# Kernel tuning notes

Hardware: AMD Instinct MI355X
Metric: run time of the kernel (lower is better)

Reference implementation:

```python
import jax, jax.numpy as jnp
import numpy as np

DIM = 1024
HEADS = 16
HEAD_DIM = DIM // HEADS
B, S, L0, L1 = 2, 2048, 2048, 2048


def setup_inputs() -> dict:
    key = jax.random.key(0)
    ks = jax.random.split(key, 10)
    sc = DIM ** -0.5
    return {
        "query": jax.random.normal(ks[0], (B, S, DIM), jnp.float32),
        "l0_keys": jax.random.normal(ks[1], (B, L0, DIM), jnp.float32),
        "l0_values": jax.random.normal(ks[2], (B, L0, DIM), jnp.float32),
        "l1_keys": jax.random.normal(ks[3], (B, L1, DIM), jnp.float32),
        "l1_values": jax.random.normal(ks[4], (B, L1, DIM), jnp.float32),
        "l0_mask": jax.random.randint(ks[5], (S, L0), 0, 2, jnp.int32),
        "Wq": jax.random.normal(ks[6], (DIM, DIM), jnp.float32) * sc,
        "bq": jnp.zeros((DIM,), jnp.float32),
        "Wo": jax.random.normal(ks[7], (DIM, DIM), jnp.float32) * sc,
        "bo": jnp.zeros((DIM,), jnp.float32),
        "gate": jnp.asarray(0.0, jnp.float32),
    }


def reference(query, l0_keys, l0_values, l1_keys, l1_values, l0_mask, Wq, bq, Wo, bo, gate):
    b, s, d = query.shape
    h, hd = HEADS, HEAD_DIM
    scale = hd ** -0.5
    # q: [B,H,S,hd]
    q = (query @ Wq.T + bq).reshape(b, s, h, hd).transpose(0, 2, 1, 3)

    def attend(keys, values, mask):
        L = keys.shape[1]
        k = keys.reshape(b, L, h, hd)
        v = values.reshape(b, L, h, hd)
        scores = jnp.einsum("bhsd,blhd->bhsl", q, k) * scale
        if mask is not None:
            scores = jnp.where(mask[None, None] == 0, -jnp.inf, scores)
        w = jax.nn.softmax(scores, axis=-1)  # [B,H,S,L]
        out = jnp.einsum("bhsl,blhd->bshd", w, v)  # [B,S,H,hd]
        return out, w.mean(axis=1)

    out0, a0 = attend(l0_keys, l0_values, l0_mask)
    out1, a1 = attend(l1_keys, l1_values, None)
    g = jax.nn.sigmoid(gate)
    out = (g * out0 + (1.0 - g) * out1).reshape(b, s, d)
    out = out @ Wo.T + bo
    return out, a0, a1
```

## Files before the change

kernel.cpp:

```cpp
#include <hip/hip_runtime.h>

#define DIM   1024
#define HEADS 16
#define HD    64
#define BB    2
#define SS    2048
#define LLL   2048
#define LOG2E 1.4426950408889634f

typedef __bf16 bf16x8 __attribute__((ext_vector_type(8)));
typedef __bf16 bf16x4v __attribute__((ext_vector_type(4)));
typedef float  f32x4  __attribute__((ext_vector_type(4)));
typedef short  s16x4  __attribute__((ext_vector_type(4)));
typedef unsigned short u16;

static __device__ __forceinline__ u16 f2b(float x) {
  unsigned u = __float_as_uint(x);
  u += 0x7fffu + ((u >> 16) & 1u);
  return (u16)(u >> 16);
}
static __device__ __forceinline__ float b2f(u16 u) {
  return __uint_as_float(((unsigned)u) << 16);
}
static __device__ __forceinline__ f32x4 mfma32(bf16x8 a, bf16x8 b, f32x4 c) {
  return __builtin_amdgcn_mfma_f32_16x16x32_bf16(a, b, c, 0, 0, 0);
}

static __device__ __forceinline__ void gload_lds16(const void* g, void* lds_uniform_base) {
#if __has_builtin(__builtin_amdgcn_global_load_lds)
  __builtin_amdgcn_global_load_lds(
      (const __attribute__((address_space(1))) unsigned int*)g,
      (__attribute__((address_space(3))) unsigned int*)lds_uniform_base, 16, 0, 0);
#else
  const int l = threadIdx.x & 63;
  ((uint4*)lds_uniform_base)[l] = ((const uint4*)g)[0];
#endif
}

__global__ void prep(const float* __restrict__ a, const float* __restrict__ b,
                     const float* __restrict__ c, u16* __restrict__ da,
                     u16* __restrict__ db_, u16* __restrict__ dc,
                     const int* __restrict__ mask, unsigned* __restrict__ mbits,
                     int na4, int nb4, int ncvt) {
  int i = blockIdx.x * blockDim.x + threadIdx.x;
  if (i < ncvt) {
    const float* s; u16* d; int j = i;
    if (j < na4) { s = a; d = da; }
    else if ((j -= na4) < nb4) { s = b; d = db_; }
    else { j -= nb4; s = c; d = dc; }
    float4 f = ((const float4*)s)[j];
    ushort4 o;
    o.x = f2b(f.x); o.y = f2b(f.y); o.z = f2b(f.z); o.w = f2b(f.w);
    ((ushort4*)d)[j] = o;
  } else {
    int j = i - ncvt;
    const int* src = mask + (size_t)j * 32;
    unsigned bm = 0;
#pragma unroll
    for (int jj = 0; jj < 8; ++jj) {
      int4 m = ((const int4*)src)[jj];
      bm |= (m.x != 0 ? 1u : 0u) << (jj * 4 + 0);
      bm |= (m.y != 0 ? 1u : 0u) << (jj * 4 + 1);
      bm |= (m.z != 0 ? 1u : 0u) << (jj * 4 + 2);
      bm |= (m.w != 0 ? 1u : 0u) << (jj * 4 + 3);
    }
    mbits[j] = bm;
  }
}

__global__ __launch_bounds__(256) void pack_k(const float* __restrict__ k0,
                                              const float* __restrict__ k1,
                                              u16* __restrict__ Kfrag) {
  const float SCK = 0.125f * LOG2E;
  const int w = threadIdx.x >> 6, l = threadIdx.x & 63, g = l >> 4, li = l & 15;
  const int lt = blockIdx.x * 4 + w, h = blockIdx.y, z = blockIdx.z;
  const int lay = z >> 1, b = z & 1;
  const float* src = (lay ? k1 : k0) + (size_t)b * LLL * DIM;
  u16* dst = Kfrag + ((((size_t)z * HEADS + h) * 32 + lt) * 8) * 512;
#pragma unroll
  for (int c = 0; c < 8; ++c) {
    int mt = c >> 1, kk = c & 1;
    const float* p = &src[(size_t)(lt * 64 + mt * 16 + li) * DIM + h * 64 + kk * 32 + g * 8];
    float4 f0 = *(const float4*)p;
    float4 f1 = *(const float4*)(p + 4);
    u16 u[8] = {f2b(f0.x * SCK), f2b(f0.y * SCK), f2b(f0.z * SCK), f2b(f0.w * SCK),
                f2b(f1.x * SCK), f2b(f1.y * SCK), f2b(f1.z * SCK), f2b(f1.w * SCK)};
    *(uint4*)&dst[c * 512 + l * 8] = *(uint4*)u;
  }
}

__global__ __launch_bounds__(256) void pack_v(const float* __restrict__ v0,
                                              const float* __restrict__ v1,
                                              u16* __restrict__ Vfrag) {
  __shared__ u16 T[64][72];
  const int lt = blockIdx.x, h = blockIdx.y, z = blockIdx.z;
  const int lay = z >> 1, b = z & 1;
  const float* v = (lay ? v1 : v0) + (size_t)b * LLL * DIM;
  const int t = threadIdx.x;
  {
    int r = t >> 2, c16 = (t & 3) * 16;
    const float* src = &v[(size_t)(lt * 64 + r) * DIM + h * 64 + c16];
#pragma unroll
    for (int i = 0; i < 4; ++i) {
      float4 f = *(const float4*)&src[i * 4];
      T[r][c16 + i * 4 + 0] = f2b(f.x);
      T[r][c16 + i * 4 + 1] = f2b(f.y);
      T[r][c16 + i * 4 + 2] = f2b(f.z);
      T[r][c16 + i * 4 + 3] = f2b(f.w);
    }
  }
  __syncthreads();
  u16* dst = Vfrag + ((((size_t)z * HEADS + h) * 32 + lt) * 8) * 512;
  {
    int lane = t & 63, g = lane >> 4, li = lane & 15;
#pragma unroll
    for (int cc = 0; cc < 2; ++cc) {
      int c = (t >> 6) + cc * 4;
      int pair = c >> 2, dt = c & 3;
      u16 u[8];
#pragma unroll
      for (int j = 0; j < 4; ++j) u[j]     = T[pair * 32 + 4 * g + j][dt * 16 + li];
#pragma unroll
      for (int j = 0; j < 4; ++j) u[4 + j] = T[pair * 32 + 16 + 4 * g + j][dt * 16 + li];
      *(uint4*)&dst[c * 512 + lane * 8] = *(uint4*)u;
    }
  }
}

template<int MODE>
__global__ __launch_bounds__(256) void gemm_nt(const u16* __restrict__ A,
                                               const u16* __restrict__ Bt,
                                               const float* __restrict__ bias,
                                               void* __restrict__ Cv,
                                               int M, int N, int K) {
  __shared__ u16 As[2][128][64];
  __shared__ u16 Bs[2][64][64];
  const int t = threadIdx.x;
  const int w = t >> 6, l = t & 63, g = l >> 4, li = l & 15;
  const int m0 = blockIdx.y * 128, n0 = blockIdx.x * 64;
  const int slotL = w * 64 + l;
  const int rA = slotL >> 3, cA = ((slotL & 7) * 8) ^ ((rA & 7) * 8);

  auto stageAB = [&](int buf, int kt) {
#pragma unroll
    for (int s = 0; s < 4; ++s) {
      int r = rA + s * 32;
      gload_lds16(&A[(size_t)(m0 + r) * K + kt + cA], &As[buf][0][0] + (s * 256 + w * 64) * 8);
    }
#pragma unroll
    for (int s = 0; s < 2; ++s) {
      int r = rA + s * 32;
      gload_lds16(&Bt[(size_t)(n0 + r) * K + kt + cA], &Bs[buf][0][0] + (s * 256 + w * 64) * 8);
    }
  };

  f32x4 acc[2][4] = {};
  stageAB(0, 0);
  __syncthreads();
  int cur = 0;
  for (int kt = 0; kt < K; kt += 64) {
    if (kt + 64 < K) stageAB(cur ^ 1, kt + 64);
#pragma unroll
    for (int kk = 0; kk < 2; ++kk) {
      bf16x8 a[2], bfr[4];
#pragma unroll
      for (int mi = 0; mi < 2; ++mi) {
        int ra = w * 32 + mi * 16 + li;
        a[mi] = *(const bf16x8*)&As[cur][ra][(kk * 32 + g * 8) ^ ((ra & 7) << 3)];
      }
#pragma unroll
      for (int ni = 0; ni < 4; ++ni) {
        int rb = ni * 16 + li;
        bfr[ni] = *(const bf16x8*)&Bs[cur][rb][(kk * 32 + g * 8) ^ ((rb & 7) << 3)];
      }
#pragma unroll
      for (int mi = 0; mi < 2; ++mi)
#pragma unroll
        for (int ni = 0; ni < 4; ++ni)
          acc[mi][ni] = mfma32(a[mi], bfr[ni], acc[mi][ni]);
    }
    __syncthreads();
    cur ^= 1;
  }
#pragma unroll
  for (int mi = 0; mi < 2; ++mi)
#pragma unroll
    for (int ni = 0; ni < 4; ++ni)
#pragma unroll
      for (int v = 0; v < 4; ++v) {
        int rr = m0 + w * 32 + mi * 16 + g * 4 + v;
        int cc = n0 + ni * 16 + li;
        float val = acc[mi][ni][v] + bias[cc];
        if (MODE == 1) {
          ((float*)Cv)[(size_t)rr * N + cc] = val;
        } else {
          int b = rr >> 11, q = rr & 2047;
          int qt = q >> 5, n = (q >> 4) & 1, liq = q & 15;
          int h = (cc >> 6) & 15, kk2 = (cc >> 5) & 1, gp = (cc >> 3) & 3, j = cc & 7;
          size_t base = ((((size_t)b * HEADS + h) * 64 + qt) * 4 + n * 2 + kk2) * 512;
          ((u16*)Cv)[base + (size_t)(gp * 16 + liq) * 8 + j] = f2b(val);
        }
      }
}

template<int MASKED>
static __device__ __forceinline__ void attn_pv_body(int z, int h, int qt, int w, int l,
                                                    const u16* __restrict__ Qfrag,
                                                    const u16* __restrict__ Kfrag,
                                                    const u16* __restrict__ Vfrag,
                                                    const unsigned* __restrict__ mbits,
                                                    u16* __restrict__ out01,
                                                    float* __restrict__ db,
                                                    u16* __restrict__ KV) {
  const int g = l >> 4, li = l & 15;
  const int b = z & 1;
  const u16* kfh = Kfrag + (size_t)(z * HEADS + h) * (32 * 8 * 512);
  const u16* vfh = Vfrag + (size_t)(z * HEADS + h) * (32 * 8 * 512);
  const u16* qfh = Qfrag + (((size_t)(b * HEADS + h) * 64 + qt) * 4) * 512;

  bf16x8 qf[2][2];
#pragma unroll
  for (int n = 0; n < 2; ++n)
#pragma unroll
    for (int kk = 0; kk < 2; ++kk)
      qf[n][kk] = *(const bf16x8*)&qfh[(n * 2 + kk) * 512 + l * 8];

  const unsigned* mrow0 = MASKED ? mbits + (size_t)(qt * 32 + li) * (LLL / 32) : nullptr;
  const unsigned* mrow1 = MASKED ? mrow0 + 16 * (LLL / 32) : nullptr;
  const int shb = 4 * g;
  bf16x8 ones8;
#pragma unroll
  for (int j = 0; j < 8; ++j) ones8[j] = __builtin_bit_cast(__bf16, (u16)0x3F80);

  auto stage = [&](int buf, int lt) {
    const u16* kfl = kfh + (size_t)lt * 4096;
    const u16* vfl = vfh + (size_t)lt * 4096;
#pragma unroll
    for (int i2 = 0; i2 < 2; ++i2) {
      int f = w * 2 + i2;
      const u16* gsrc = (f < 8 ? kfl + f * 512 : vfl + (f - 8) * 512) + l * 8;
      gload_lds16(gsrc, (char*)KV + buf * 16384 + f * 1024);
    }
  };

  f32x4 dacc[2] = {};
  f32x4 oacc[4][2] = {};

  stage(0, 0);
  __syncthreads();
  int cur = 0;
  for (int lt = 0; lt < 32; ++lt) {
    if (lt + 1 < 32) stage(cur ^ 1, lt + 1);
    unsigned mw[2][2];
    if (MASKED) {
      mw[0][0] = mrow0[lt * 2]; mw[0][1] = mrow0[lt * 2 + 1];
      mw[1][0] = mrow1[lt * 2]; mw[1][1] = mrow1[lt * 2 + 1];
    }
    const u16* Ks = KV + cur * 8192;
    const u16* Vs = Ks + 4096;

    auto qk = [&](f32x4 (&s)[2], int mt) {
      bf16x8 k0 = *(const bf16x8*)&Ks[(mt * 2 + 0) * 512 + l * 8];
      bf16x8 k1 = *(const bf16x8*)&Ks[(mt * 2 + 1) * 512 + l * 8];
      f32x4 zz = {};
      __builtin_amdgcn_s_setprio(1);
      s[0] = mfma32(k0, qf[0][0], zz);
      s[0] = mfma32(k1, qf[0][1], s[0]);
      s[1] = mfma32(k0, qf[1][0], zz);
      s[1] = mfma32(k1, qf[1][1], s[1]);
      __builtin_amdgcn_s_setprio(0);
    };
    auto sm = [&](f32x4 (&s)[2], int mt, s16x4 (&wpk)[2]) {
#pragma unroll
      for (int n = 0; n < 2; ++n) {
        unsigned mm = MASKED ? (mw[n][mt >> 1] >> ((mt & 1) * 16 + shb)) : 0u;
        f32x4 ev;
#pragma unroll
        for (int v = 0; v < 4; ++v) {
          float e = __builtin_amdgcn_exp2f(s[n][v]);
          if (MASKED) {
            int spread = ((int)(mm << (31 - v))) >> 31;
            e = __uint_as_float(__float_as_uint(e) & (unsigned)spread);
          }
          ev[v] = e;
        }
        bf16x4v wb = __builtin_convertvector(ev, bf16x4v);
        wpk[n] = __builtin_bit_cast(s16x4, wb);
      }
    };
    auto pv_pair = [&](s16x4 (&w0)[2], s16x4 (&w1)[2], int pair) {
      bf16x8 w8[2];
#pragma unroll
      for (int n = 0; n < 2; ++n) {
        bf16x4v a0 = __builtin_bit_cast(bf16x4v, w0[n]);
        bf16x4v a1 = __builtin_bit_cast(bf16x4v, w1[n]);
        w8[n] = __builtin_shufflevector(a0, a1, 0, 1, 2, 3, 4, 5, 6, 7);
      }
      __builtin_amdgcn_s_setprio(1);
      dacc[0] = mfma32(ones8, w8[0], dacc[0]);
      dacc[1] = mfma32(ones8, w8[1], dacc[1]);
#pragma unroll
      for (int dt = 0; dt < 4; ++dt) {
        bf16x8 vf = *(const bf16x8*)&Vs[(pair * 4 + dt) * 512 + l * 8];
#pragma unroll
        for (int n = 0; n < 2; ++n)
          oacc[dt][n] = mfma32(vf, w8[n], oacc[dt][n]);
      }
      __builtin_amdgcn_s_setprio(0);
    };

    f32x4 sA[2], sB[2];
    s16x4 wA[2], wB[2];
    qk(sA, 0); qk(sB, 1);
    sm(sA, 0, wA);
    qk(sA, 2);
    sm(sB, 1, wB);
    pv_pair(wA, wB, 0);
    qk(sB, 3);
    sm(sA, 2, wA);
    sm(sB, 3, wB);
    pv_pair(wA, wB, 1);
    __syncthreads();
    cur ^= 1;
  }
  float dinv[2];
  dinv[0] = 1.0f / dacc[0][0];
  dinv[1] = 1.0f / dacc[1][0];
  if (l < 16) {
    db[(size_t)(z * HEADS + h) * SS + qt * 32 + li]      = -__log2f(dacc[0][0]);
    db[(size_t)(z * HEADS + h) * SS + qt * 32 + 16 + li] = -__log2f(dacc[1][0]);
  }
  u16* ob = out01 + (size_t)z * SS * DIM;
#pragma unroll
  for (int dt = 0; dt < 4; ++dt)
#pragma unroll
    for (int n = 0; n < 2; ++n) {
      f32x4 o = oacc[dt][n] * dinv[n];
      ushort4 us;
      us.x = f2b(o[0]); us.y = f2b(o[1]); us.z = f2b(o[2]); us.w = f2b(o[3]);
      *(ushort4*)&ob[((size_t)(qt * 32 + n * 16 + li)) * DIM + h * HD + dt * 16 + 4 * g] = us;
    }
}

__global__ __launch_bounds__(512, 4) void attn_pv(const u16* __restrict__ Qfrag,
                                                  const u16* __restrict__ Kfrag,
                                                  const u16* __restrict__ Vfrag,
                                                  const unsigned* __restrict__ mbits,
                                                  u16* __restrict__ out01,
                                                  float* __restrict__ db) {
  __shared__ u16 KV[2][8192];
  const int flat = blockIdx.x;
  const int xcd = flat & 7, i = flat >> 3;
  const int k = i >> 3, qg = i & 7;
  const int zh = xcd + 8 * k;
  const int z = zh >> 4, h = zh & 15;
  const int w = threadIdx.x >> 6, l = threadIdx.x & 63;
  const int qt = qg * 8 + w;
  if (z < 2) attn_pv_body<1>(z, h, qt, w, l, Qfrag, Kfrag, Vfrag, mbits, out01, db, &KV[0][0]);
  else       attn_pv_body<0>(z, h, qt, w, l, Qfrag, Kfrag, Vfrag, mbits, out01, db, &KV[0][0]);
}

template<int MASKED>
static __device__ __forceinline__ void amean_body(int z, int qt, int lt, int w, int l,
                                                  const u16* __restrict__ Qfrag,
                                                  const u16* __restrict__ Kfrag,
                                                  const unsigned* __restrict__ mbits,
                                                  const float* __restrict__ db,
                                                  float* __restrict__ aout,
                                                  u16* __restrict__ KS) {
  const int g = l >> 4, li = l & 15;
  const int b = z & 1;

  unsigned mw[2][2];
  if (MASKED) {
    const unsigned* m0 = mbits + (size_t)(qt * 32 + li) * (LLL / 32) + lt * 2;
    const unsigned* m1 = m0 + 16 * (LLL / 32);
    mw[0][0] = m0[0]; mw[0][1] = m0[1];
    mw[1][0] = m1[0]; mw[1][1] = m1[1];
  }
  const u16* qf_base = Qfrag + (((size_t)(b * HEADS) * 64 + qt) * 4) * 512 + l * 8;
  const float* dbb = db + (size_t)(z * HEADS) * SS + qt * 32 + li;

  auto stageK = [&](int buf, int h) {
    const u16* kfh = Kfrag + ((((size_t)(z * HEADS + h)) * 32 + lt) * 8) * 512;
    gload_lds16(kfh + w * 512 + l * 8, (char*)KS + buf * 8192 + w * 1024);
  };

  f32x4 asum[4][2] = {};
  stageK(0, 0);
  __syncthreads();
#pragma unroll 2
  for (int h = 0; h < HEADS; ++h) {
    if (h + 1 < HEADS) stageK((h + 1) & 1, h + 1);
    float l2[2];
    l2[0] = dbb[(size_t)h * SS];
    l2[1] = dbb[(size_t)h * SS + 16];
    bf16x8 qf[2][2];
#pragma unroll
    for (int n = 0; n < 2; ++n)
#pragma unroll
      for (int kk = 0; kk < 2; ++kk)
        qf[n][kk] = *(const bf16x8*)&qf_base[(size_t)h * (64 * 4 * 512) + (n * 2 + kk) * 512];
    const u16* Ks = KS + (h & 1) * 4096;
#pragma unroll
    for (int mt = 0; mt < 4; ++mt) {
      bf16x8 k0 = *(const bf16x8*)&Ks[(mt * 2 + 0) * 512 + l * 8];
      bf16x8 k1 = *(const bf16x8*)&Ks[(mt * 2 + 1) * 512 + l * 8];
#pragma unroll
      for (int n = 0; n < 2; ++n) {
        f32x4 s;
        __builtin_amdgcn_s_setprio(1);
        f32x4 zz = {};
        s = mfma32(k0, qf[n][0], zz);
        s = mfma32(k1, qf[n][1], s);
        __builtin_amdgcn_s_setprio(0);
        unsigned mm = MASKED ? (mw[n][mt >> 1] >> ((mt & 1) * 16 + 4 * g)) : 0u;
#pragma unroll
        for (int v = 0; v < 4; ++v) {
          float e = __builtin_amdgcn_exp2f(s[v] + l2[n]);
          if (MASKED) {
            int spread = ((int)(mm << (31 - v))) >> 31;
            e = __uint_as_float(__float_as_uint(e) & (unsigned)spread);
          }
          asum[mt][n][v] += e;
        }
      }
    }
    __syncthreads();
  }
  float* ab = aout + (size_t)z * SS * LLL;
#pragma unroll
  for (int mt = 0; mt < 4; ++mt)
#pragma unroll
    for (int n = 0; n < 2; ++n) {
      f32x4 o = asum[mt][n] * 0.0625f;
      f32x4* dst = (f32x4*)&ab[(size_t)(qt * 32 + n * 16 + li) * LLL + lt * 64 + mt * 16 + 4 * g];
      __builtin_nontemporal_store(o, dst);
    }
}

__global__ __launch_bounds__(512, 4) void amean(const u16* __restrict__ Qfrag,
                                                const u16* __restrict__ Kfrag,
                                                const unsigned* __restrict__ mbits,
                                                const float* __restrict__ db,
                                                float* __restrict__ aout) {
  __shared__ u16 KS[2][4096];
  const int flat = blockIdx.x;
  const int xcd = flat & 7, i = flat >> 3;
  const int k = i >> 3, qg = i & 7;
  const int zlt = xcd + 8 * k;
  const int z = zlt >> 5, lt = zlt & 31;
  const int w = threadIdx.x >> 6, l = threadIdx.x & 63;
  const int qt = qg * 8 + w;
  if (z < 2) amean_body<1>(z, qt, lt, w, l, Qfrag, Kfrag, mbits, db, aout, &KS[0][0]);
  else       amean_body<0>(z, qt, lt, w, l, Qfrag, Kfrag, mbits, db, aout, &KS[0][0]);
}

__global__ void merge_kernel(const u16* __restrict__ o01,
                             const float* __restrict__ gate,
                             u16* __restrict__ merged) {
  int i = blockIdx.x * blockDim.x + threadIdx.x;
  float gv = gate[0];
  float g = 1.0f / (1.0f + __builtin_amdgcn_exp2f(-gv * LOG2E));
  const size_t n = (size_t)BB * SS * DIM;
  ushort4 a = ((const ushort4*)o01)[i];
  ushort4 c = ((const ushort4*)(o01 + n))[i];
  ushort4 o;
  o.x = f2b(g * b2f(a.x) + (1.f - g) * b2f(c.x));
  o.y = f2b(g * b2f(a.y) + (1.f - g) * b2f(c.y));
  o.z = f2b(g * b2f(a.z) + (1.f - g) * b2f(c.z));
  o.w = f2b(g * b2f(a.w) + (1.f - g) * b2f(c.w));
  ((ushort4*)merged)[i] = o;
}

extern "C" void kernel_launch(void* const* d_in, const int* in_sizes, int n_in,
                              void* d_out, int out_size, void* d_ws, size_t ws_size,
                              hipStream_t stream) {
  const float* query = (const float*)d_in[0];
  const float* k0f   = (const float*)d_in[1];
  const float* v0f   = (const float*)d_in[2];
  const float* k1f   = (const float*)d_in[3];
  const float* v1f   = (const float*)d_in[4];
  const int*   mask  = (const int*)d_in[5];
  const float* Wqf   = (const float*)d_in[6];
  const float* bq    = (const float*)d_in[7];
  const float* Wof   = (const float*)d_in[8];
  const float* bo    = (const float*)d_in[9];
  const float* gate  = (const float*)d_in[10];
  float* out = (float*)d_out;

  const size_t nQ = (size_t)BB * SS * DIM;
  const size_t nW = (size_t)DIM * DIM;

  char* ws = (char*)d_ws;
  size_t off = 0;
  auto alloc = [&](size_t bytes) -> char* {
    char* p = ws + off;
    off += (bytes + 255) & ~(size_t)255;
    return p;
  };
  u16*      queryb  = (u16*)alloc(nQ * 2);
  u16*      wqb     = (u16*)alloc(nW * 2);
  u16*      wob     = (u16*)alloc(nW * 2);
  u16*      Qfrag   = (u16*)alloc(nQ * 2);
  u16*      Kfrag   = (u16*)alloc((size_t)2 * nQ * 2);
  u16*      Vfrag   = (u16*)alloc((size_t)2 * nQ * 2);
  unsigned* mbits   = (unsigned*)alloc((size_t)SS * (LLL / 32) * 4);
  float*    db      = (float*)alloc((size_t)4 * HEADS * SS * 4);
  u16*      out01   = (u16*)alloc((size_t)2 * nQ * 2);
  u16*      mergedb = queryb;

  {
    int na4 = (int)(nQ / 4), nb4 = (int)(nW / 4);
    int ncvt = na4 + 2 * nb4;
    int nmask = SS * (LLL / 32);
    prep<<<dim3((ncvt + nmask) / 256), dim3(256), 0, stream>>>(
        query, Wqf, Wof, queryb, wqb, wob, mask, mbits, na4, nb4, ncvt);
  }

  pack_k<<<dim3(LLL / 64 / 4, HEADS, 4), dim3(256), 0, stream>>>(k0f, k1f, Kfrag);
  pack_v<<<dim3(LLL / 64, HEADS, 4), dim3(256), 0, stream>>>(v0f, v1f, Vfrag);

  gemm_nt<2><<<dim3(DIM / 64, (BB * SS) / 128), dim3(256), 0, stream>>>(
      queryb, wqb, bq, (void*)Qfrag, BB * SS, DIM, DIM);

  attn_pv<<<dim3(512), dim3(512), 0, stream>>>(Qfrag, Kfrag, Vfrag, mbits, out01, db);

  amean<<<dim3(1024), dim3(512), 0, stream>>>(Qfrag, Kfrag, mbits, db, out + nQ);

  merge_kernel<<<dim3((int)(nQ / 4 / 256)), dim3(256), 0, stream>>>(out01, gate, mergedb);

  gemm_nt<1><<<dim3(DIM / 64, (BB * SS) / 128), dim3(256), 0, stream>>>(
      mergedb, wob, bo, (void*)out, BB * SS, DIM, DIM);
}
```

Before: 213.1 us.

## Simplify amean softmax: store reciprocal denom, mask once at store, smaller blocks

The attention kernel now stores the reciprocal of the softmax denominator instead of a negative log2, so amean computes exp2(s)*dinv with an FMA instead of adding a bias inside the exp. Because the mask is the same for every head, it is applied once to the final mean at store time rather than per head inside the loop. The mask-word registers and setprio calls are dropped. amean also moves to 256-thread blocks with twice as many blocks, each wave staging two K fragments, to change occupancy and scheduling.

```diff
diff --git a/kernel.cpp b/kernel.cpp
--- a/kernel.cpp
+++ b/kernel.cpp
@@ -327,8 +327,8 @@
   dinv[0] = 1.0f / dacc[0][0];
   dinv[1] = 1.0f / dacc[1][0];
   if (l < 16) {
-    db[(size_t)(z * HEADS + h) * SS + qt * 32 + li]      = -__log2f(dacc[0][0]);
-    db[(size_t)(z * HEADS + h) * SS + qt * 32 + 16 + li] = -__log2f(dacc[1][0]);
+    db[(size_t)(z * HEADS + h) * SS + qt * 32 + li]      = dinv[0];
+    db[(size_t)(z * HEADS + h) * SS + qt * 32 + 16 + li] = dinv[1];
   }
   u16* ob = out01 + (size_t)z * SS * DIM;
 #pragma unroll
@@ -371,19 +371,16 @@
   const int g = l >> 4, li = l & 15;
   const int b = z & 1;
 
-  unsigned mw[2][2];
-  if (MASKED) {
-    const unsigned* m0 = mbits + (size_t)(qt * 32 + li) * (LLL / 32) + lt * 2;
-    const unsigned* m1 = m0 + 16 * (LLL / 32);
-    mw[0][0] = m0[0]; mw[0][1] = m0[1];
-    mw[1][0] = m1[0]; mw[1][1] = m1[1];
-  }
   const u16* qf_base = Qfrag + (((size_t)(b * HEADS) * 64 + qt) * 4) * 512 + l * 8;
   const float* dbb = db + (size_t)(z * HEADS) * SS + qt * 32 + li;
 
   auto stageK = [&](int buf, int h) {
     const u16* kfh = Kfrag + ((((size_t)(z * HEADS + h)) * 32 + lt) * 8) * 512;
-    gload_lds16(kfh + w * 512 + l * 8, (char*)KS + buf * 8192 + w * 1024);
+#pragma unroll
+    for (int i2 = 0; i2 < 2; ++i2) {
+      int f = w * 2 + i2;
+      gload_lds16(kfh + f * 512 + l * 8, (char*)KS + buf * 8192 + f * 1024);
+    }
   };
 
   f32x4 asum[4][2] = {};
@@ -392,9 +389,9 @@
 #pragma unroll 2
   for (int h = 0; h < HEADS; ++h) {
     if (h + 1 < HEADS) stageK((h + 1) & 1, h + 1);
-    float l2[2];
-    l2[0] = dbb[(size_t)h * SS];
-    l2[1] = dbb[(size_t)h * SS + 16];
+    float dv[2];
+    dv[0] = dbb[(size_t)h * SS];
+    dv[1] = dbb[(size_t)h * SS + 16];
     bf16x8 qf[2][2];
 #pragma unroll
     for (int n = 0; n < 2; ++n)
@@ -408,22 +405,12 @@
       bf16x8 k1 = *(const bf16x8*)&Ks[(mt * 2 + 1) * 512 + l * 8];
 #pragma unroll
       for (int n = 0; n < 2; ++n) {
-        f32x4 s;
-        __builtin_amdgcn_s_setprio(1);
-        f32x4 zz = {};
-        s = mfma32(k0, qf[n][0], zz);
+        f32x4 s = {};
+        s = mfma32(k0, qf[n][0], s);
         s = mfma32(k1, qf[n][1], s);
-        __builtin_amdgcn_s_setprio(0);
-        unsigned mm = MASKED ? (mw[n][mt >> 1] >> ((mt & 1) * 16 + 4 * g)) : 0u;
-#pragma unroll
-        for (int v = 0; v < 4; ++v) {
-          float e = __builtin_amdgcn_exp2f(s[v] + l2[n]);
-          if (MASKED) {
-            int spread = ((int)(mm << (31 - v))) >> 31;
-            e = __uint_as_float(__float_as_uint(e) & (unsigned)spread);
-          }
-          asum[mt][n][v] += e;
-        }
+#pragma unroll
+        for (int v = 0; v < 4; ++v)
+          asum[mt][n][v] = __builtin_fmaf(__builtin_amdgcn_exp2f(s[v]), dv[n], asum[mt][n][v]);
       }
     }
     __syncthreads();
@@ -434,12 +421,21 @@
 #pragma unroll
     for (int n = 0; n < 2; ++n) {
       f32x4 o = asum[mt][n] * 0.0625f;
+      if (MASKED) {
+        const unsigned* mrow = mbits + (size_t)(qt * 32 + n * 16 + li) * (LLL / 32) + lt * 2;
+        unsigned mm = mrow[mt >> 1] >> ((mt & 1) * 16 + 4 * g);
+#pragma unroll
+        for (int v = 0; v < 4; ++v) {
+          int spread = ((int)(mm << (31 - v))) >> 31;
+          o[v] = __uint_as_float(__float_as_uint(o[v]) & (unsigned)spread);
+        }
+      }
       f32x4* dst = (f32x4*)&ab[(size_t)(qt * 32 + n * 16 + li) * LLL + lt * 64 + mt * 16 + 4 * g];
       __builtin_nontemporal_store(o, dst);
     }
 }
 
-__global__ __launch_bounds__(512, 4) void amean(const u16* __restrict__ Qfrag,
+__global__ __launch_bounds__(256, 4) void amean(const u16* __restrict__ Qfrag,
                                                 const u16* __restrict__ Kfrag,
                                                 const unsigned* __restrict__ mbits,
                                                 const float* __restrict__ db,
@@ -447,11 +443,11 @@
   __shared__ u16 KS[2][4096];
   const int flat = blockIdx.x;
   const int xcd = flat & 7, i = flat >> 3;
-  const int k = i >> 3, qg = i & 7;
+  const int k = i >> 4, qg = i & 15;
   const int zlt = xcd + 8 * k;
   const int z = zlt >> 5, lt = zlt & 31;
   const int w = threadIdx.x >> 6, l = threadIdx.x & 63;
-  const int qt = qg * 8 + w;
+  const int qt = qg * 4 + w;
   if (z < 2) amean_body<1>(z, qt, lt, w, l, Qfrag, Kfrag, mbits, db, aout, &KS[0][0]);
   else       amean_body<0>(z, qt, lt, w, l, Qfrag, Kfrag, mbits, db, aout, &KS[0][0]);
 }
@@ -526,7 +522,7 @@
 
   attn_pv<<<dim3(512), dim3(512), 0, stream>>>(Qfrag, Kfrag, Vfrag, mbits, out01, db);
 
-  amean<<<dim3(1024), dim3(512), 0, stream>>>(Qfrag, Kfrag, mbits, db, out + nQ);
+  amean<<<dim3(2048), dim3(256), 0, stream>>>(Qfrag, Kfrag, mbits, db, out + nQ);
 
   merge_kernel<<<dim3((int)(nQ / 4 / 256)), dim3(256), 0, stream>>>(out01, gate, mergedb);
 
```

Measured after the change: 209.1 us. Within noise of the previous version (-1.9%).
